# Kernel optimization log

Measured on AMD Instinct MI355X. Metric: run time of the kernel, lower is better.

The kernel has to match this reference:

```python
import jax, jax.numpy as jnp
import numpy as np
from jax import lax

NCLASSES = 3
NMS_PRE = 100
NMS_THR = 0.01
SCORE_THR = 0.1
MAX_NUM = 50
H, W = 248, 216
BS = 16


def make_anchors():
    # Faithful to Anchors(ranges, sizes, rotations) in __init__.
    z0s = np.array([-0.6, -0.6, -1.78], np.float32)
    sizes = np.array([[0.6, 0.8, 1.73], [0.6, 1.76, 1.73], [1.6, 3.9, 1.56]], np.float32)
    rotations = np.array([0.0, 1.57], np.float32)
    x = (np.arange(W, dtype=np.float32) + 0.5) * (69.12 / W)
    y = (np.arange(H, dtype=np.float32) + 0.5) * (79.36 / H) - 39.68
    yy, xx = np.meshgrid(y, x, indexing='ij')  # (H, W)
    anchors = np.zeros((H, W, 3, 2, 7), np.float32)
    for c in range(3):
        for r in range(2):
            anchors[:, :, c, r, 0] = xx
            anchors[:, :, c, r, 1] = yy
            anchors[:, :, c, r, 2] = z0s[c]
            anchors[:, :, c, r, 3:6] = sizes[c]
            anchors[:, :, c, r, 6] = rotations[r]
    return jnp.asarray(anchors)


def setup_inputs() -> dict:
    key = jax.random.key(0)
    k1, k2, k3 = jax.random.split(key, 3)
    return {
        'bbox_cls_pred': jax.random.normal(k1, (BS, 18, H, W), jnp.float32),
        'bbox_pred': jax.random.normal(k2, (BS, 42, H, W), jnp.float32) * 0.1,
        'bbox_dir_cls_pred': jax.random.normal(k3, (BS, 12, H, W), jnp.float32),
        'anchors': make_anchors(),
    }


def limit_period(val, offset=1.0, period=np.pi):
    return val - jnp.floor(val / period + offset) * period


def anchors2bboxes(anchors, deltas):
    xa, ya, za, wa, la, ha, ra = [anchors[:, i] for i in range(7)]
    dx, dy, dz, dw, dl, dh, dr = [deltas[:, i] for i in range(7)]
    da = jnp.sqrt(wa * wa + la * la)
    x = dx * da + xa
    y = dy * da + ya
    z = dz * ha + za + ha * 0.5
    w = wa * jnp.exp(dw)
    l = la * jnp.exp(dl)
    h = ha * jnp.exp(dh)
    z = z - h * 0.5
    theta = ra + dr
    return jnp.stack([x, y, z, w, l, h, theta], axis=-1)


def nms_keep(boxes2d, scores, valid, thresh):
    # Greedy NMS over fixed NMS_PRE boxes; invalid boxes never kept / never suppress.
    n = scores.shape[0]
    order = jnp.argsort(-jnp.where(valid, scores, -jnp.inf))
    b = boxes2d[order]
    v = valid[order]
    area = (b[:, 2] - b[:, 0]) * (b[:, 3] - b[:, 1])
    x1 = jnp.maximum(b[:, None, 0], b[None, :, 0])
    y1 = jnp.maximum(b[:, None, 1], b[None, :, 1])
    x2 = jnp.minimum(b[:, None, 2], b[None, :, 2])
    y2 = jnp.minimum(b[:, None, 3], b[None, :, 3])
    inter = jnp.maximum(x2 - x1, 0.0) * jnp.maximum(y2 - y1, 0.0)
    iou = inter / (area[:, None] + area[None, :] - inter + 1e-8)
    idx = jnp.arange(n)
    def body(i, keep):
        sup = (iou[i] > thresh) & (idx > i) & keep[i]
        return keep & ~sup
    keep = lax.fori_loop(0, n, body, v)
    return jnp.zeros(n, bool).at[order].set(keep)


def process_single(cls_pred, box_pred, dir_pred, anchors):
    # cls_pred (18,H,W), box_pred (42,H,W), dir_pred (12,H,W), anchors (H,W,3,2,7)
    cls = jnp.transpose(cls_pred, (1, 2, 0)).reshape(-1, NCLASSES)
    box = jnp.transpose(box_pred, (1, 2, 0)).reshape(-1, 7)
    dirp = jnp.transpose(dir_pred, (1, 2, 0)).reshape(-1, 2)
    anc = anchors.reshape(-1, 7)
    cls = jax.nn.sigmoid(cls)
    dir_cls = jnp.argmax(dirp, axis=1)
    _, inds = lax.top_k(jnp.max(cls, axis=1), NMS_PRE)
    cls = cls[inds]
    box = box[inds]
    dir_cls = dir_cls[inds]
    anc = anc[inds]
    bboxes = anchors2bboxes(anc, box)  # (NMS_PRE, 7): x,y,z,w,l,h,theta
    xy = bboxes[:, :2]
    wl = bboxes[:, 3:5]
    boxes2d = jnp.concatenate([xy - wl / 2, xy + wl / 2], axis=-1)
    # Torch code detaches theta through limit_period; dir term is constant.
    theta = lax.stop_gradient(limit_period(bboxes[:, 6])) + (1.0 - dir_cls.astype(bboxes.dtype)) * np.pi
    bboxes = bboxes.at[:, 6].set(theta)
    keeps = []
    for c in range(NCLASSES):
        sc = cls[:, c]
        valid = sc > SCORE_THR
        keeps.append(nms_keep(boxes2d, sc, valid, NMS_THR) & valid)
    keep = jnp.stack(keeps)            # (3, NMS_PRE)
    scores_all = cls.T                 # (3, NMS_PRE)
    flat = jnp.where(keep, scores_all, -1.0).reshape(-1)
    final_scores, fi = lax.top_k(flat, MAX_NUM)
    sel = fi % NMS_PRE
    labels = fi // NMS_PRE
    out_bboxes = bboxes[sel]
    mask = final_scores > 0.0
    return out_bboxes, labels, final_scores, mask


def reference(bbox_cls_pred, bbox_pred, bbox_dir_cls_pred, anchors):
    f = jax.vmap(process_single, in_axes=(0, 0, 0, None))
    return f(bbox_cls_pred, bbox_pred, bbox_dir_cls_pred, anchors)
```

## Files before the change

kernel.cpp:

```cpp
#include <hip/hip_runtime.h>
#include <cstdint>

#pragma clang fp contract(off)

#define HH 248
#define WW 216
#define HW (HH*WW)
#define BATCH 16
#define NPRE 100
#define MAXNUM 50
#define NB 2048
#define CAP 2048
#define SBLK 53
#define PIF 3.14159274101257324f

#define CNT_OFF  0
#define TB_OFF   64
#define KEYS_OFF 128
#define SH_OFF   (KEYS_OFF + BATCH*CAP*8)

__device__ __forceinline__ float sigmoidf_ref(float x) {
    if (x >= 0.0f) {
        return 1.0f / (1.0f + expf(-x));
    } else {
        float e = expf(x);
        return e / (1.0f + e);
    }
}

__global__ __launch_bounds__(256) void k_score(const float* __restrict__ cls,
                                               unsigned short* __restrict__ subhist) {
    int t = threadIdx.x, blk = blockIdx.x, b = blockIdx.y;
    __shared__ unsigned hist[NB];
    for (int i = t; i < NB; i += 256) hist[i] = 0;
    __syncthreads();

    int cell0 = blk * 1024 + t * 4;
    if (cell0 < HW) {
        const float* p = cls + (size_t)b * 18 * HW;
        for (int a = 0; a < 6; ++a) {
            float4 l0 = *(const float4*)(p + (size_t)(a*3+0)*HW + cell0);
            float4 l1 = *(const float4*)(p + (size_t)(a*3+1)*HW + cell0);
            float4 l2 = *(const float4*)(p + (size_t)(a*3+2)*HW + cell0);
            float m0 = fmaxf(l0.x, fmaxf(l1.x, l2.x));
            float m1 = fmaxf(l0.y, fmaxf(l1.y, l2.y));
            float m2 = fmaxf(l0.z, fmaxf(l1.z, l2.z));
            float m3 = fmaxf(l0.w, fmaxf(l1.w, l2.w));
            atomicAdd(&hist[__float_as_uint(sigmoidf_ref(m0)) >> 19], 1u);
            atomicAdd(&hist[__float_as_uint(sigmoidf_ref(m1)) >> 19], 1u);
            atomicAdd(&hist[__float_as_uint(sigmoidf_ref(m2)) >> 19], 1u);
            atomicAdd(&hist[__float_as_uint(sigmoidf_ref(m3)) >> 19], 1u);
        }
    }
    __syncthreads();
    unsigned short* sh = subhist + (size_t)(b * SBLK + blk) * NB;
    for (int i = t; i < NB; i += 256) sh[i] = (unsigned short)hist[i];
}

__global__ __launch_bounds__(256) void k_reduce(const unsigned short* __restrict__ subhist,
                                                unsigned* __restrict__ tbo) {
    int b = blockIdx.x, t = threadIdx.x;
    __shared__ unsigned h[NB];
    const unsigned short* base = subhist + (size_t)b * SBLK * NB;
    for (int j = t; j < NB; j += 256) {
        unsigned s = 0;
        for (int k = 0; k < SBLK; ++k) s += base[(size_t)k * NB + j];
        h[j] = s;
    }
    __syncthreads();
    if (t == 0) {
        unsigned cum = 0;
        int r = NB - 1;
        for (; r >= 0; --r) { cum += h[r]; if (cum >= NPRE) break; }
        tbo[b] = (unsigned)(r < 0 ? 0 : r);
    }
}

__global__ __launch_bounds__(256) void k_collect(const float* __restrict__ cls,
                                                 const unsigned* __restrict__ tbo,
                                                 unsigned* __restrict__ cnt,
                                                 unsigned long long* __restrict__ keys) {
    int t = threadIdx.x, blk = blockIdx.x, b = blockIdx.y;
    int cell0 = blk * 1024 + t * 4;
    if (cell0 >= HW) return;
    unsigned tb = tbo[b];
    const float* p = cls + (size_t)b * 18 * HW;
    for (int a = 0; a < 6; ++a) {
        float4 l0 = *(const float4*)(p + (size_t)(a*3+0)*HW + cell0);
        float4 l1 = *(const float4*)(p + (size_t)(a*3+1)*HW + cell0);
        float4 l2 = *(const float4*)(p + (size_t)(a*3+2)*HW + cell0);
        float m[4];
        m[0] = fmaxf(l0.x, fmaxf(l1.x, l2.x));
        m[1] = fmaxf(l0.y, fmaxf(l1.y, l2.y));
        m[2] = fmaxf(l0.z, fmaxf(l1.z, l2.z));
        m[3] = fmaxf(l0.w, fmaxf(l1.w, l2.w));
        for (int e = 0; e < 4; ++e) {
            unsigned bits = __float_as_uint(sigmoidf_ref(m[e]));
            if ((bits >> 19) >= tb) {
                unsigned pos = atomicAdd(&cnt[b], 1u);
                if (pos < CAP) {
                    unsigned row = (unsigned)((cell0 + e) * 6 + a);
                    keys[(size_t)b * CAP + pos] =
                        ((unsigned long long)bits << 32) |
                        (unsigned long long)(0xFFFFFFFFu - row);
                }
            }
        }
    }
}

__global__ __launch_bounds__(256) void k_final(
    const float* __restrict__ cls, const float* __restrict__ box,
    const float* __restrict__ dir, const float* __restrict__ anc,
    const unsigned* __restrict__ cnt, const unsigned long long* __restrict__ keys,
    float* __restrict__ out) {
    int b = blockIdx.x, t = threadIdx.x;

    __shared__ unsigned long long keyS[CAP];
    __shared__ int   selRow[NPRE];
    __shared__ float bb[NPRE][7];
    __shared__ float b2d[NPRE][4];
    __shared__ float areaS[NPRE];
    __shared__ float clsS[3][NPRE];
    __shared__ float svalS[3][NPRE];
    __shared__ int   ordS[3][NPRE];
    __shared__ int   rankS[3][NPRE];
    __shared__ unsigned keepInit[3][4];
    __shared__ unsigned long long maskS[3][NPRE][2];
    __shared__ unsigned long long keepBits[3][2];
    __shared__ float flatS[3*NPRE];

    unsigned cn = cnt[b];
    int M = (cn < (unsigned)CAP) ? (int)cn : CAP;
    for (int i = t; i < CAP; i += 256)
        keyS[i] = (i < M) ? keys[(size_t)b * CAP + i] : 0ULL;
    __syncthreads();

    for (int i = t; i < M; i += 256) {
        unsigned long long k = keyS[i];
        int r = 0;
        for (int j = 0; j < M; ++j) r += (keyS[j] > k);
        if (r < NPRE) selRow[r] = (int)(0xFFFFFFFFu - (unsigned)(k & 0xFFFFFFFFull));
    }
    __syncthreads();

    if (t < NPRE) {
        int row = selRow[t];
        int a = row % 6;
        int cell = row / 6;
        const float* cb = cls + (size_t)b * 18 * HW + cell;
        clsS[0][t] = sigmoidf_ref(cb[(size_t)(a*3+0)*HW]);
        clsS[1][t] = sigmoidf_ref(cb[(size_t)(a*3+1)*HW]);
        clsS[2][t] = sigmoidf_ref(cb[(size_t)(a*3+2)*HW]);
        const float* db = dir + (size_t)b * 12 * HW + cell;
        float d0 = db[(size_t)(a*2+0)*HW];
        float d1 = db[(size_t)(a*2+1)*HW];
        int dircls = (d1 > d0) ? 1 : 0;
        const float* pb = box + (size_t)b * 42 * HW + cell;
        float dx = pb[(size_t)(a*7+0)*HW], dy = pb[(size_t)(a*7+1)*HW], dz = pb[(size_t)(a*7+2)*HW];
        float dw = pb[(size_t)(a*7+3)*HW], dl = pb[(size_t)(a*7+4)*HW], dh = pb[(size_t)(a*7+5)*HW];
        float dr = pb[(size_t)(a*7+6)*HW];
        const float* ab = anc + (size_t)row * 7;
        float xa = ab[0], ya = ab[1], za = ab[2];
        float wa = ab[3], la = ab[4], ha = ab[5], ra = ab[6];
        float da = sqrtf(wa*wa + la*la);
        float x = dx*da + xa;
        float y = dy*da + ya;
        float z = dz*ha + za + ha*0.5f;
        float wv = wa*expf(dw);
        float lv = la*expf(dl);
        float hv = ha*expf(dh);
        z = z - hv*0.5f;
        float th0 = ra + dr;
        float lim = th0 - floorf(th0/PIF + 1.0f)*PIF;
        float theta = lim + (1.0f - (float)dircls)*PIF;
        bb[t][0]=x; bb[t][1]=y; bb[t][2]=z; bb[t][3]=wv; bb[t][4]=lv; bb[t][5]=hv; bb[t][6]=theta;
        b2d[t][0] = x - wv*0.5f;
        b2d[t][1] = y - lv*0.5f;
        b2d[t][2] = x + wv*0.5f;
        b2d[t][3] = y + lv*0.5f;
        areaS[t] = (b2d[t][2]-b2d[t][0]) * (b2d[t][3]-b2d[t][1]);
    }
    if (t < 12) keepInit[t/4][t%4] = 0u;
    __syncthreads();

    for (int w = t; w < 3*NPRE; w += 256) {
        int c = w / NPRE, p = w % NPRE;
        float sc = clsS[c][p];
        svalS[c][p] = (sc > 0.1f) ? sc : -INFINITY;
    }
    __syncthreads();

    for (int w = t; w < 3*NPRE; w += 256) {
        int c = w / NPRE, p = w % NPRE;
        float v = svalS[c][p];
        int r = 0;
        for (int j = 0; j < NPRE; ++j) {
            float vj = svalS[c][j];
            if (vj > v || (vj == v && j < p)) ++r;
        }
        ordS[c][r] = p;
        rankS[c][p] = r;
        if (v != -INFINITY) atomicOr(&keepInit[c][r >> 5], 1u << (r & 31));
    }
    __syncthreads();

    for (int w = t; w < 3*NPRE; w += 256) {
        int c = w / NPRE, i = w % NPRE;
        int pi = ordS[c][i];
        unsigned long long m0 = 0ULL, m1 = 0ULL;
        float ax1 = b2d[pi][0], ay1 = b2d[pi][1], ax2 = b2d[pi][2], ay2 = b2d[pi][3];
        float ai = areaS[pi];
        for (int j = i + 1; j < NPRE; ++j) {
            int pj = ordS[c][j];
            float x1 = fmaxf(ax1, b2d[pj][0]);
            float y1 = fmaxf(ay1, b2d[pj][1]);
            float x2 = fminf(ax2, b2d[pj][2]);
            float y2 = fminf(ay2, b2d[pj][3]);
            float inter = fmaxf(x2 - x1, 0.0f) * fmaxf(y2 - y1, 0.0f);
            float iou = inter / (ai + areaS[pj] - inter + 1e-8f);
            if (iou > 0.01f) {
                if (j < 64) m0 |= (1ULL << j);
                else        m1 |= (1ULL << (j - 64));
            }
        }
        maskS[c][i][0] = m0;
        maskS[c][i][1] = m1;
    }
    __syncthreads();

    if (t < 3) {
        int c = t;
        unsigned long long k0 = (unsigned long long)keepInit[c][0] |
                                ((unsigned long long)keepInit[c][1] << 32);
        unsigned long long k1 = (unsigned long long)keepInit[c][2] |
                                ((unsigned long long)keepInit[c][3] << 32);
        for (int i = 0; i < NPRE; ++i) {
            unsigned long long bit = (i < 64) ? (k0 >> i) : (k1 >> (i - 64));
            if (bit & 1ULL) {
                k0 &= ~maskS[c][i][0];
                k1 &= ~maskS[c][i][1];
            }
        }
        keepBits[c][0] = k0;
        keepBits[c][1] = k1;
    }
    __syncthreads();

    for (int w = t; w < 3*NPRE; w += 256) {
        int c = w / NPRE, p = w % NPRE;
        int r = rankS[c][p];
        unsigned long long bit = (r < 64) ? (keepBits[c][0] >> r) : (keepBits[c][1] >> (r - 64));
        flatS[w] = (bit & 1ULL) ? clsS[c][p] : -1.0f;
    }
    __syncthreads();

    for (int i = t; i < 3*NPRE; i += 256) {
        float vi = flatS[i];
        int r2 = 0;
        for (int j = 0; j < 3*NPRE; ++j) {
            float vj = flatS[j];
            if (vj > vi || (vj == vi && j < i)) ++r2;
        }
        if (r2 < MAXNUM) {
            int p = i % NPRE;
            int lab = i / NPRE;
            int o = b * MAXNUM + r2;
            float* ob = out + (size_t)o * 7;
            for (int j = 0; j < 7; ++j) ob[j] = bb[p][j];
            out[BATCH*MAXNUM*7 + o] = (float)lab;
            out[BATCH*MAXNUM*8 + o] = vi;
            out[BATCH*MAXNUM*9 + o] = (vi > 0.0f) ? 1.0f : 0.0f;
        }
    }
}

extern "C" void kernel_launch(void* const* d_in, const int* in_sizes, int n_in,
                              void* d_out, int out_size, void* d_ws, size_t ws_size,
                              hipStream_t stream) {
    const float* cls = (const float*)d_in[0];
    const float* box = (const float*)d_in[1];
    const float* dir = (const float*)d_in[2];
    const float* anc = (const float*)d_in[3];
    float* out = (float*)d_out;
    char* ws = (char*)d_ws;

    unsigned* cnt = (unsigned*)(ws + CNT_OFF);
    unsigned* tb  = (unsigned*)(ws + TB_OFF);
    unsigned long long* keys = (unsigned long long*)(ws + KEYS_OFF);
    unsigned short* subhist  = (unsigned short*)(ws + SH_OFF);

    hipMemsetAsync(cnt, 0, 64, stream);

    dim3 g(SBLK, BATCH);
    k_score  <<<g, 256, 0, stream>>>(cls, subhist);
    k_reduce <<<BATCH, 256, 0, stream>>>(subhist, tb);
    k_collect<<<g, 256, 0, stream>>>(cls, tb, cnt, keys);
    k_final  <<<BATCH, 256, 0, stream>>>(cls, box, dir, anc, cnt, keys, out);
}
```

Measured before the change: 362.1 us.

## Cache per-anchor score bits and refine histogram buckets for top-k threshold

The scoring pass now writes the per-anchor max-sigmoid bits to workspace, so the collect pass reads one value per anchor instead of re-reading all 18 logit channels and recomputing sigmoids. The histogram grows to 4096 buckets, with finer resolution for scores above 0.5, to tighten the candidate threshold. The threshold search becomes a two-level scan. The scoring grid shrinks to 14 blocks per batch, each looping over 4 chunks, which cuts partial-histogram traffic but leaves fewer blocks to hide memory latency on a bandwidth-bound pass.

After: 352.7 us. -2.6%, faster.

```diff
diff --git a/kernel.cpp b/kernel.cpp
--- a/kernel.cpp
+++ b/kernel.cpp
@@ -6,18 +6,22 @@
 #define HH 248
 #define WW 216
 #define HW (HH*WW)
+#define NROW (6*HW)
 #define BATCH 16
 #define NPRE 100
 #define MAXNUM 50
-#define NB 2048
+#define NB 4096
 #define CAP 2048
-#define SBLK 53
+#define CPB 4096
+#define SBLK 14
+#define CBLK 314
 #define PIF 3.14159274101257324f
 
 #define CNT_OFF  0
 #define TB_OFF   64
 #define KEYS_OFF 128
 #define SH_OFF   (KEYS_OFF + BATCH*CAP*8)
+#define SB_OFF   (SH_OFF + BATCH*SBLK*NB*2)
 
 __device__ __forceinline__ float sigmoidf_ref(float x) {
     if (x >= 0.0f) {
@@ -28,28 +32,41 @@
     }
 }
 
+__device__ __forceinline__ unsigned bucket_of(unsigned bits) {
+    unsigned b = (bits >= 0x3F000000u) ? (2048u + ((bits - 0x3F000000u) >> 12))
+                                       : (bits >> 19);
+    return (b > (unsigned)(NB - 1)) ? (unsigned)(NB - 1) : b;
+}
+
 __global__ __launch_bounds__(256) void k_score(const float* __restrict__ cls,
+                                               unsigned* __restrict__ sb,
                                                unsigned short* __restrict__ subhist) {
     int t = threadIdx.x, blk = blockIdx.x, b = blockIdx.y;
     __shared__ unsigned hist[NB];
     for (int i = t; i < NB; i += 256) hist[i] = 0;
     __syncthreads();
 
-    int cell0 = blk * 1024 + t * 4;
-    if (cell0 < HW) {
-        const float* p = cls + (size_t)b * 18 * HW;
-        for (int a = 0; a < 6; ++a) {
-            float4 l0 = *(const float4*)(p + (size_t)(a*3+0)*HW + cell0);
-            float4 l1 = *(const float4*)(p + (size_t)(a*3+1)*HW + cell0);
-            float4 l2 = *(const float4*)(p + (size_t)(a*3+2)*HW + cell0);
-            float m0 = fmaxf(l0.x, fmaxf(l1.x, l2.x));
-            float m1 = fmaxf(l0.y, fmaxf(l1.y, l2.y));
-            float m2 = fmaxf(l0.z, fmaxf(l1.z, l2.z));
-            float m3 = fmaxf(l0.w, fmaxf(l1.w, l2.w));
-            atomicAdd(&hist[__float_as_uint(sigmoidf_ref(m0)) >> 19], 1u);
-            atomicAdd(&hist[__float_as_uint(sigmoidf_ref(m1)) >> 19], 1u);
-            atomicAdd(&hist[__float_as_uint(sigmoidf_ref(m2)) >> 19], 1u);
-            atomicAdd(&hist[__float_as_uint(sigmoidf_ref(m3)) >> 19], 1u);
+    const float* p = cls + (size_t)b * 18 * HW;
+    unsigned* sbb = sb + (size_t)b * NROW;
+
+    for (int k = 0; k < 4; ++k) {
+        int cell0 = blk * CPB + k * 1024 + t * 4;
+        if (cell0 < HW) {
+            for (int a = 0; a < 6; ++a) {
+                float4 l0 = *(const float4*)(p + (size_t)(a*3+0)*HW + cell0);
+                float4 l1 = *(const float4*)(p + (size_t)(a*3+1)*HW + cell0);
+                float4 l2 = *(const float4*)(p + (size_t)(a*3+2)*HW + cell0);
+                unsigned b0 = __float_as_uint(sigmoidf_ref(fmaxf(l0.x, fmaxf(l1.x, l2.x))));
+                unsigned b1 = __float_as_uint(sigmoidf_ref(fmaxf(l0.y, fmaxf(l1.y, l2.y))));
+                unsigned b2 = __float_as_uint(sigmoidf_ref(fmaxf(l0.z, fmaxf(l1.z, l2.z))));
+                unsigned b3 = __float_as_uint(sigmoidf_ref(fmaxf(l0.w, fmaxf(l1.w, l2.w))));
+                atomicAdd(&hist[bucket_of(b0)], 1u);
+                atomicAdd(&hist[bucket_of(b1)], 1u);
+                atomicAdd(&hist[bucket_of(b2)], 1u);
+                atomicAdd(&hist[bucket_of(b3)], 1u);
+                uint4 v; v.x = b0; v.y = b1; v.z = b2; v.w = b3;
+                *(uint4*)(sbb + (size_t)a*HW + cell0) = v;
+            }
         }
     }
     __syncthreads();
@@ -61,6 +78,7 @@
                                                 unsigned* __restrict__ tbo) {
     int b = blockIdx.x, t = threadIdx.x;
     __shared__ unsigned h[NB];
+    __shared__ unsigned csum[256];
     const unsigned short* base = subhist + (size_t)b * SBLK * NB;
     for (int j = t; j < NB; j += 256) {
         unsigned s = 0;
@@ -68,42 +86,50 @@
         h[j] = s;
     }
     __syncthreads();
+    unsigned cs = 0;
+    for (int q = 0; q < 16; ++q) cs += h[t * 16 + q];
+    csum[t] = cs;
+    __syncthreads();
     if (t == 0) {
         unsigned cum = 0;
-        int r = NB - 1;
-        for (; r >= 0; --r) { cum += h[r]; if (cum >= NPRE) break; }
-        tbo[b] = (unsigned)(r < 0 ? 0 : r);
-    }
-}
-
-__global__ __launch_bounds__(256) void k_collect(const float* __restrict__ cls,
+        int r = 0;
+        for (int u = 255; u >= 0; --u) {
+            if (cum + csum[u] >= NPRE) {
+                unsigned c2 = cum;
+                for (int k2 = (u + 1) * 16 - 1; k2 >= u * 16; --k2) {
+                    c2 += h[k2];
+                    if (c2 >= NPRE) { r = k2; break; }
+                }
+                break;
+            }
+            cum += csum[u];
+        }
+        tbo[b] = (unsigned)r;
+    }
+}
+
+__global__ __launch_bounds__(256) void k_collect(const unsigned* __restrict__ sb,
                                                  const unsigned* __restrict__ tbo,
                                                  unsigned* __restrict__ cnt,
                                                  unsigned long long* __restrict__ keys) {
     int t = threadIdx.x, blk = blockIdx.x, b = blockIdx.y;
-    int cell0 = blk * 1024 + t * 4;
-    if (cell0 >= HW) return;
+    int i0 = blk * 1024 + t * 4;
+    if (i0 >= NROW) return;
     unsigned tb = tbo[b];
-    const float* p = cls + (size_t)b * 18 * HW;
-    for (int a = 0; a < 6; ++a) {
-        float4 l0 = *(const float4*)(p + (size_t)(a*3+0)*HW + cell0);
-        float4 l1 = *(const float4*)(p + (size_t)(a*3+1)*HW + cell0);
-        float4 l2 = *(const float4*)(p + (size_t)(a*3+2)*HW + cell0);
-        float m[4];
-        m[0] = fmaxf(l0.x, fmaxf(l1.x, l2.x));
-        m[1] = fmaxf(l0.y, fmaxf(l1.y, l2.y));
-        m[2] = fmaxf(l0.z, fmaxf(l1.z, l2.z));
-        m[3] = fmaxf(l0.w, fmaxf(l1.w, l2.w));
-        for (int e = 0; e < 4; ++e) {
-            unsigned bits = __float_as_uint(sigmoidf_ref(m[e]));
-            if ((bits >> 19) >= tb) {
-                unsigned pos = atomicAdd(&cnt[b], 1u);
-                if (pos < CAP) {
-                    unsigned row = (unsigned)((cell0 + e) * 6 + a);
-                    keys[(size_t)b * CAP + pos] =
-                        ((unsigned long long)bits << 32) |
-                        (unsigned long long)(0xFFFFFFFFu - row);
-                }
+    uint4 v = *(const uint4*)(sb + (size_t)b * NROW + i0);
+    unsigned bs[4] = {v.x, v.y, v.z, v.w};
+    for (int e = 0; e < 4; ++e) {
+        unsigned bits = bs[e];
+        if (bucket_of(bits) >= tb) {
+            unsigned pos = atomicAdd(&cnt[b], 1u);
+            if (pos < CAP) {
+                int i = i0 + e;
+                int a = i / HW;
+                int cell = i - a * HW;
+                unsigned row = (unsigned)(cell * 6 + a);
+                keys[(size_t)b * CAP + pos] =
+                    ((unsigned long long)bits << 32) |
+                    (unsigned long long)(0xFFFFFFFFu - row);
             }
         }
     }
@@ -289,12 +315,14 @@
     unsigned* tb  = (unsigned*)(ws + TB_OFF);
     unsigned long long* keys = (unsigned long long*)(ws + KEYS_OFF);
     unsigned short* subhist  = (unsigned short*)(ws + SH_OFF);
+    unsigned* sb             = (unsigned*)(ws + SB_OFF);
 
     hipMemsetAsync(cnt, 0, 64, stream);
 
-    dim3 g(SBLK, BATCH);
-    k_score  <<<g, 256, 0, stream>>>(cls, subhist);
+    dim3 gs(SBLK, BATCH);
+    dim3 gc(CBLK, BATCH);
+    k_score  <<<gs, 256, 0, stream>>>(cls, sb, subhist);
     k_reduce <<<BATCH, 256, 0, stream>>>(subhist, tb);
-    k_collect<<<g, 256, 0, stream>>>(cls, tb, cnt, keys);
+    k_collect<<<gc, 256, 0, stream>>>(sb, tb, cnt, keys);
     k_final  <<<BATCH, 256, 0, stream>>>(cls, box, dir, anc, cnt, keys, out);
 }
```
